# Optimization experiments

Measured on AMD Instinct MI355X. Metric: run time of the kernel, lower is better.

The kernel has to match this reference:

```python
import jax, jax.numpy as jnp
import numpy as np

BLOCK_SIZE = 4
CHANNEL_USE = 7
SAMPS = 20  # samps_per_symb in the original forward
LEAK = 0.01  # nn.LeakyReLU default slope


def _make_filters(K=101):
    # Deterministic stand-ins for h_lowpass.txt / h_pulseshape.txt
    n = np.arange(K) - (K - 1) / 2
    fc = 1.0 / SAMPS
    h_lp = (np.sinc(2 * fc * n) * np.hamming(K) * 2 * fc).astype(np.float32)
    h_ps = (np.sinc(n / SAMPS) * np.hamming(K)).astype(np.float32)
    return h_lp, h_ps


def _conv_same(sig, h):
    # Batched equivalent of np.convolve(row, h, 'same') for odd-length h.
    # sig: [N, L] float, h: [K] float. True convolution => flip kernel for lax correlation.
    K = h.shape[0]
    pad = (K - 1) // 2
    out = jax.lax.conv_general_dilated(
        sig[:, None, :], h[::-1][None, None, :],
        window_strides=(1,), padding=[(pad, pad)],
        dimension_numbers=('NCH', 'OIH', 'NCH'))
    return out[:, 0, :]


def setup_inputs() -> dict:
    key = jax.random.key(0)
    B, IN, CD = 131072, 16, 7
    ks = jax.random.split(key, 6)

    def lin(k, fi, fo):
        bound = 1.0 / np.sqrt(fi)
        kw, kb = jax.random.split(k)
        W = jax.random.uniform(kw, (fo, fi), jnp.float32, -bound, bound)
        b = jax.random.uniform(kb, (fo,), jnp.float32, -bound, bound)
        return W, b

    We1, be1 = lin(ks[0], IN, IN)
    We2, be2 = lin(ks[1], IN, CD)
    Wd1, bd1 = lin(ks[2], CD, IN)
    Wd2, bd2 = lin(ks[3], IN, IN)
    x = jax.random.normal(ks[4], (B, IN), jnp.float32)
    noise = jax.random.normal(ks[5], (B, CD), jnp.float32)
    h_lp, h_ps = _make_filters()
    return dict(x=x, We1=We1, be1=be1, We2=We2, be2=be2,
                Wd1=Wd1, bd1=bd1, Wd2=Wd2, bd2=bd2,
                h_lowpass=jnp.asarray(h_lp), h_pulseshape=jnp.asarray(h_ps),
                noise=noise, snr=4)


def reference(x, We1, be1, We2, be2, Wd1, bd1, Wd2, bd2,
              h_lowpass, h_pulseshape, noise, snr):
    B = x.shape[0]
    # ---- encoder MLP + global-norm scaling to power 70 ----
    h = jnp.dot(x, We1.T) + be1
    h = jnp.where(h >= 0, h, LEAK * h)
    enc = jnp.dot(h, We2.T) + be2
    enc = enc / jnp.linalg.norm(enc) * 70.0

    CD = enc.shape[1]          # bits_per_code
    M = 2 ** CD                # PSK order

    # ---- non-differentiable PSK channel (torch does .cpu().detach()) ----
    e = jax.lax.stop_gradient(enc)
    xi = jnp.round(e).astype(jnp.int32)           # int(np.round(.)) per element
    sign = jnp.where(xi < 0, -1.0, 1.0)           # sign_mask
    idx = jnp.mod(jnp.abs(xi), M)                  # bin() drops sign; values < M in practice
    phase = (2.0 * jnp.pi / M) * idx.astype(jnp.float32)
    sr, si = jnp.cos(phase), jnp.sin(phase)        # commpy PSK constellation exp(2*pi*i/M)

    def up(s):  # zero-stuff upsample by SAMPS: [B, CD] -> [B, CD*SAMPS]
        u = jnp.zeros((B, CD, SAMPS), s.dtype).at[:, :, 0].set(s)
        return u.reshape(B, CD * SAMPS)

    sig = jnp.concatenate([up(sr), up(si)], axis=0)  # real/imag stacked: [2B, L]
    sig = _conv_same(sig, h_pulseshape)
    sig = _conv_same(sig, h_lowpass)
    sig = _conv_same(sig, h_pulseshape)
    y = sig[:, ::SAMPS] * SAMPS                      # downsample, [2B, CD]
    yr, yi = y[:B], y[B:]
    # hard PSK demod = nearest unit-circle point = phase quantization
    ang = jnp.arctan2(yi, yr)
    idx_hat = jnp.mod(jnp.round(ang * (M / (2.0 * jnp.pi))), M)
    res = idx_hat.astype(jnp.float32) * sign

    # ---- AWGN ----
    rate = BLOCK_SIZE / CHANNEL_USE
    snr_lin = 10.0 ** (0.1 * snr)
    res = res + noise / jnp.sqrt(jnp.float32(2.0 * rate * snr_lin))

    # ---- decoder MLP ----
    d = jnp.dot(res, Wd1.T) + bd1
    d = jnp.where(d >= 0, d, LEAK * d)
    out = jnp.dot(d, Wd2.T) + bd2
    return out
```

## Files before the change

### kernel.cpp

```cpp
#include <hip/hip_runtime.h>
#include <math.h>

#define IN_DIM   16
#define CD       7
#define SAMPS    20
#define KFILT    101
#define SIGLEN   140
#define MCONST   128


__device__ __forceinline__ unsigned ld_u32(const void* p) {
    return __hip_atomic_load((const unsigned*)p, __ATOMIC_RELAXED,
                             __HIP_MEMORY_SCOPE_AGENT);
}
__device__ __forceinline__ void st_u32(void* p, unsigned v) {
    __hip_atomic_store((unsigned*)p, v, __ATOMIC_RELAXED,
                       __HIP_MEMORY_SCOPE_AGENT);
}
__device__ __forceinline__ unsigned add_u32(void* p) {
    return __hip_atomic_fetch_add((unsigned*)p, 1u, __ATOMIC_RELAXED,
                                  __HIP_MEMORY_SCOPE_AGENT);
}
__device__ __forceinline__ double ld_f64(const void* p) {
    return __hip_atomic_load((const double*)p, __ATOMIC_RELAXED,
                             __HIP_MEMORY_SCOPE_AGENT);
}
__device__ __forceinline__ void st_f64(void* p, double v) {
    __hip_atomic_store((double*)p, v, __ATOMIC_RELAXED,
                       __HIP_MEMORY_SCOPE_AGENT);
}
__device__ __forceinline__ float ld_f32(const void* p) {
    return __hip_atomic_load((const float*)p, __ATOMIC_RELAXED,
                             __HIP_MEMORY_SCOPE_AGENT);
}
__device__ __forceinline__ void st_f32(void* p, float v) {
    __hip_atomic_store((float*)p, v, __ATOMIC_RELAXED,
                       __HIP_MEMORY_SCOPE_AGENT);
}

__global__ __launch_bounds__(256, 2) void k_fused(
    const float* __restrict__ x,
    const float* __restrict__ We1, const float* __restrict__ be1,
    const float* __restrict__ We2, const float* __restrict__ be2,
    const float* __restrict__ Wd1, const float* __restrict__ bd1,
    const float* __restrict__ Wd2, const float* __restrict__ bd2,
    const float* __restrict__ h_lp, const float* __restrict__ h_ps,
    const float* __restrict__ noise, const int* __restrict__ snr_p,
    char* __restrict__ ws, float* __restrict__ out, int B, int NB)
{
    int t   = threadIdx.x;
    int bid = blockIdx.x;
    int row = bid * 256 + t;

    double* partials = (double*)(ws + 0);
    float*  GR       = (float*) (ws + 4096);
    char*   L0       = ws + 8192;
    char*   GS       = ws + 10240;
    char*   ROOT     = ws + 12288;
    char*   FLAG     = ws + 12544;

    __shared__ float    sW1[256], sW2[112], sb1[16], sb2[7];
    __shared__ float    sV1[112], sV2[256], sc1[16], sc2[16];
    __shared__ float    str[2 * MCONST];
    __shared__ float    snz[256 * CD];
    __shared__ double   wred[4];
    __shared__ float    sG[49];
    __shared__ float    curp[240], nxtp[240];
    __shared__ float    hA[KFILT], hB[KFILT];
    __shared__ unsigned sNormBits;
    __shared__ float    ninv;

    sW1[t] = We1[t];  sV2[t] = Wd2[t];
    if (t < 112) { sW2[t] = We2[t]; sV1[t] = Wd1[t]; }
    if (t < 16)  { sb1[t] = be1[t]; sc1[t] = bd1[t]; sc2[t] = bd2[t]; }
    if (t < 7)   sb2[t] = be2[t];
    if (bid < CD && t < KFILT) { hA[t] = h_ps[t]; hB[t] = h_lp[t]; }
    if (t < MCONST) {
        float ph = (float)(2.0 * 3.14159265358979323846 / (double)MCONST) * (float)t;
        str[t]          = cosf(ph);
        str[MCONST + t] = sinf(ph);
    }
    __syncthreads();

    float e[CD];
    double ss = 0.0;
    if (row < B) {
        const float4* xp = reinterpret_cast<const float4*>(x + (size_t)row * IN_DIM);
        float4 v0 = xp[0], v1 = xp[1], v2 = xp[2], v3 = xp[3];
        float xr[16] = {v0.x,v0.y,v0.z,v0.w, v1.x,v1.y,v1.z,v1.w,
                        v2.x,v2.y,v2.z,v2.w, v3.x,v3.y,v3.z,v3.w};
        float h[16];
        #pragma unroll
        for (int i = 0; i < 16; ++i) {
            float acc = sb1[i];
            #pragma unroll
            for (int j = 0; j < 16; ++j) acc = fmaf(sW1[i*16+j], xr[j], acc);
            h[i] = (acc >= 0.f) ? acc : 0.01f * acc;
        }
        #pragma unroll
        for (int o = 0; o < CD; ++o) {
            float acc = sb2[o];
            #pragma unroll
            for (int i = 0; i < 16; ++i) acc = fmaf(sW2[o*16+i], h[i], acc);
            e[o] = acc;
            ss += (double)acc * (double)acc;
        }
    }
    double v = ss;
    #pragma unroll
    for (int off = 32; off > 0; off >>= 1) v += __shfl_down(v, off);
    if ((t & 63) == 0) wred[t >> 6] = v;
    __syncthreads();
    if (t == 0) st_f64(&partials[bid], (wred[0] + wred[1]) + (wred[2] + wred[3]));

    if (bid < CD) {
        if (t < 240) { curp[t] = 0.0f; nxtp[t] = 0.0f; }
        __syncthreads();
        if (t < SIGLEN) {
            int m = t + 50 - SAMPS * bid;
            curp[t + 50] = (m >= 0 && m < KFILT) ? hA[m] : 0.0f;
        }
        __syncthreads();
        for (int f = 0; f < 2; ++f) {
            const float* h = (f == 0) ? hB : hA;
            if (t < SIGLEN) {
                float a0 = 0.f, a1 = 0.f;
                for (int m = 0; m <= 50; ++m)    a0 = fmaf(h[m], curp[t + 100 - m], a0);
                for (int m = 51; m < KFILT; ++m) a1 = fmaf(h[m], curp[t + 100 - m], a1);
                nxtp[t + 50] = a0 + a1;
            }
            __syncthreads();
            if (t < SIGLEN) curp[t + 50] = nxtp[t + 50];
            __syncthreads();
        }
        if (t < CD) {
            float gv = (float)SAMPS * curp[t * SAMPS + 50];
            #pragma unroll
            for (int r = 0; r < 8; ++r)
                st_f32(&GR[r * 64 + t * CD + bid], gv);
        }
    }

    {
        size_t nb  = (size_t)bid * (256 * CD);
        size_t lim = (size_t)B * CD;
        for (int i = t; i < 256 * CD; i += 256)
            if (nb + i < lim) snz[i] = noise[nb + i];
    }
    if (t == 1) {
        int iv = *snr_p;
        float sv = (iv >= -1000 && iv <= 1000) ? (float)iv
                                               : *reinterpret_cast<const float*>(snr_p);
        float snr_lin = powf(10.0f, 0.1f * sv);
        ninv = 1.0f / sqrtf((float)(8.0 / 7.0) * snr_lin);
    }

    __syncthreads();
    if (t < 64) {
        asm volatile("s_waitcnt vmcnt(0)" ::: "memory");
        int g       = bid >> 6;
        int gbase   = g << 6;
        int gsize   = (NB - gbase < 64) ? (NB - gbase) : 64;
        int ngroups = (NB + 63) >> 6;

        unsigned aret = 0;
        if (t == 0) aret = add_u32(L0 + (size_t)g * 256);
        aret = __shfl(aret, 0);
        if ((int)aret == gsize - 1) {
            double p = (t < gsize) ? ld_f64(&partials[gbase + t]) : 0.0;
            #pragma unroll
            for (int off = 32; off > 0; off >>= 1) p += __shfl_down(p, off);
            unsigned rret = 0;
            if (t == 0) {
                st_f64(GS + (size_t)g * 256, p);
                asm volatile("s_waitcnt vmcnt(0)" ::: "memory");
                rret = add_u32(ROOT);
            }
            rret = __shfl(rret, 0);
            if ((int)rret == ngroups - 1) {
                double gsv = (t < ngroups) ? ld_f64(GS + (size_t)t * 256) : 0.0;
                #pragma unroll
                for (int off = 32; off > 0; off >>= 1) gsv += __shfl_down(gsv, off);
                unsigned bits = 0;
                if (t == 0) bits = __float_as_uint((float)sqrt(gsv));
                bits = __shfl(bits, 0);
                if (t < 8) st_u32(FLAG + (size_t)t * 256, bits);
            }
        }
        if (t == 0) {
            unsigned b2;
            while ((b2 = ld_u32(FLAG + (size_t)(bid & 7) * 256)) == 0u)
                __builtin_amdgcn_s_sleep(4);
            sNormBits = b2;
        }
        if (t < 49) sG[t] = ld_f32(&GR[(size_t)(bid & 7) * 64 + t]);
    }
    __syncthreads();
    float sinv = 70.0f / __uint_as_float(sNormBits);

    if (row >= B) return;

    float sr[CD], si[CD], sgn[CD];
    #pragma unroll
    for (int o = 0; o < CD; ++o) {
        float es = e[o] * sinv;
        float rv = rintf(es);
        int xi = (int)rv;
        sgn[o] = (xi < 0) ? -1.0f : 1.0f;
        int idx = (xi < 0 ? -xi : xi) & (MCONST - 1);
        sr[o] = str[idx];
        si[o] = str[MCONST + idx];
    }

    float res[CD];
    #pragma unroll
    for (int k = 0; k < CD; ++k) {
        float yr = 0.f, yi = 0.f;
        #pragma unroll
        for (int cc = 0; cc < CD; ++cc) {
            float g = sG[k * CD + cc];
            yr = fmaf(g, sr[cc], yr);
            yi = fmaf(g, si[cc], yi);
        }
        float ang = atan2f(yi, yr);
        float q = ang * (float)(128.0 / (2.0 * 3.14159265358979323846));
        float r = rintf(q);
        float m = (r < 0.0f) ? r + 128.0f : r;
        res[k] = fmaf(snz[t * CD + k], ninv, m * sgn[k]);
    }

    float dd[16];
    #pragma unroll
    for (int i = 0; i < 16; ++i) {
        float acc = sc1[i];
        #pragma unroll
        for (int cc = 0; cc < CD; ++cc) acc = fmaf(sV1[i*CD+cc], res[cc], acc);
        dd[i] = (acc >= 0.f) ? acc : 0.01f * acc;
    }
    float4* op = reinterpret_cast<float4*>(out + (size_t)row * IN_DIM);
    #pragma unroll
    for (int q4 = 0; q4 < 4; ++q4) {
        float o0[4];
        #pragma unroll
        for (int u = 0; u < 4; ++u) {
            int i = q4 * 4 + u;
            float acc = sc2[i];
            #pragma unroll
            for (int j = 0; j < 16; ++j) acc = fmaf(sV2[i*16+j], dd[j], acc);
            o0[u] = acc;
        }
        op[q4] = make_float4(o0[0], o0[1], o0[2], o0[3]);
    }
}

__global__ __launch_bounds__(256) void k1_enc(
    const float* __restrict__ x,
    const float* __restrict__ We1, const float* __restrict__ be1,
    const float* __restrict__ We2, const float* __restrict__ be2,
    const float* __restrict__ h_lp, const float* __restrict__ h_ps,
    float* __restrict__ enc, double* __restrict__ partials,
    float* __restrict__ Gd, int B)
{
    int t = threadIdx.x, bid = blockIdx.x, row = bid * 256 + t;
    __shared__ float  sW1[256], sW2[112], sb1[16], sb2[7];
    __shared__ double wred[4];
    __shared__ float  curp[240], nxtp[240];
    __shared__ float  hA[KFILT], hB[KFILT];
    sW1[t] = We1[t];
    if (t < 112) sW2[t] = We2[t];
    if (t < 16)  sb1[t] = be1[t];
    if (t < 7)   sb2[t] = be2[t];
    if (bid < CD && t < KFILT) { hA[t] = h_ps[t]; hB[t] = h_lp[t]; }
    __syncthreads();
    double ss = 0.0;
    if (row < B) {
        const float4* xp = reinterpret_cast<const float4*>(x + (size_t)row * IN_DIM);
        float4 v0 = xp[0], v1 = xp[1], v2 = xp[2], v3 = xp[3];
        float xr[16] = {v0.x,v0.y,v0.z,v0.w, v1.x,v1.y,v1.z,v1.w,
                        v2.x,v2.y,v2.z,v2.w, v3.x,v3.y,v3.z,v3.w};
        float h[16];
        #pragma unroll
        for (int i = 0; i < 16; ++i) {
            float acc = sb1[i];
            #pragma unroll
            for (int j = 0; j < 16; ++j) acc = fmaf(sW1[i*16+j], xr[j], acc);
            h[i] = (acc >= 0.f) ? acc : 0.01f * acc;
        }
        float e[8];
        #pragma unroll
        for (int o = 0; o < CD; ++o) {
            float acc = sb2[o];
            #pragma unroll
            for (int i = 0; i < 16; ++i) acc = fmaf(sW2[o*16+i], h[i], acc);
            e[o] = acc; ss += (double)acc * (double)acc;
        }
        e[7] = 0.f;
        float4* ep = reinterpret_cast<float4*>(enc + (size_t)row * 8);
        ep[0] = make_float4(e[0], e[1], e[2], e[3]);
        ep[1] = make_float4(e[4], e[5], e[6], e[7]);
    }
    double v = ss;
    #pragma unroll
    for (int off = 32; off > 0; off >>= 1) v += __shfl_down(v, off);
    if ((t & 63) == 0) wred[t >> 6] = v;
    __syncthreads();
    if (t == 0) partials[bid] = (wred[0] + wred[1]) + (wred[2] + wred[3]);
    if (bid < CD) {
        if (t < 240) { curp[t] = 0.0f; nxtp[t] = 0.0f; }
        __syncthreads();
        if (t < SIGLEN) {
            int m = t + 50 - SAMPS * bid;
            curp[t + 50] = (m >= 0 && m < KFILT) ? hA[m] : 0.0f;
        }
        __syncthreads();
        for (int f = 0; f < 2; ++f) {
            const float* h = (f == 0) ? hB : hA;
            if (t < SIGLEN) {
                float a0 = 0.f, a1 = 0.f;
                for (int m = 0; m <= 50; ++m)    a0 = fmaf(h[m], curp[t + 100 - m], a0);
                for (int m = 51; m < KFILT; ++m) a1 = fmaf(h[m], curp[t + 100 - m], a1);
                nxtp[t + 50] = a0 + a1;
            }
            __syncthreads();
            if (t < SIGLEN) curp[t + 50] = nxtp[t + 50];
            __syncthreads();
        }
        if (t < CD) Gd[t * CD + bid] = (float)SAMPS * curp[t * SAMPS + 50];
    }
}

__global__ __launch_bounds__(256) void k2_main(
    const float* __restrict__ enc,
    const float* __restrict__ Wd1, const float* __restrict__ bd1,
    const float* __restrict__ Wd2, const float* __restrict__ bd2,
    const float* __restrict__ noise, const int* __restrict__ snr_p,
    const double* __restrict__ partials, const float* __restrict__ Gd,
    float* __restrict__ out, int B, int NBP)
{
    int t = threadIdx.x, bid = blockIdx.x, base_row = bid * 512;
    __shared__ float  sV1[112], sc1[16], sV2[256], sc2[16];
    __shared__ float  str[2 * MCONST];
    __shared__ float  sG[49];
    __shared__ double wred[4];
    __shared__ float  snz[512 * CD];
    __shared__ float  sinv, ninv;
    sV2[t] = Wd2[t];
    if (t < 112) sV1[t] = Wd1[t];
    if (t < 16)  { sc1[t] = bd1[t]; sc2[t] = bd2[t]; }
    if (t < 49)  sG[t] = Gd[t];
    if (t < MCONST) {
        float ph = (float)(2.0 * 3.14159265358979323846 / (double)MCONST) * (float)t;
        str[t] = cosf(ph); str[MCONST + t] = sinf(ph);
    }
    {
        size_t nb = (size_t)base_row * CD, lim = (size_t)B * CD;
        for (int i = t; i < 512 * CD; i += 256)
            if (nb + i < lim) snz[i] = noise[nb + i];
    }
    {
        double s = 0.0;
        for (int i = t; i < NBP; i += 256) s += partials[i];
        #pragma unroll
        for (int off = 32; off > 0; off >>= 1) s += __shfl_down(s, off);
        if ((t & 63) == 0) wred[t >> 6] = s;
    }
    __syncthreads();
    if (t == 0) sinv = 70.0f / (float)sqrt((wred[0] + wred[1]) + (wred[2] + wred[3]));
    if (t == 1) {
        int iv = *snr_p;
        float sv = (iv >= -1000 && iv <= 1000) ? (float)iv
                                               : *reinterpret_cast<const float*>(snr_p);
        float snr_lin = powf(10.0f, 0.1f * sv);
        ninv = 1.0f / sqrtf((float)(8.0 / 7.0) * snr_lin);
    }
    __syncthreads();
    #pragma unroll
    for (int c = 0; c < 2; ++c) {
        int lrow = c * 256 + t, row = base_row + lrow;
        if (row >= B) continue;
        const float4* ep = reinterpret_cast<const float4*>(enc + (size_t)row * 8);
        float4 e0 = ep[0], e1 = ep[1];
        float ev[7] = {e0.x, e0.y, e0.z, e0.w, e1.x, e1.y, e1.z};
        float sr[CD], si[CD], sgn[CD];
        #pragma unroll
        for (int o = 0; o < CD; ++o) {
            float es = ev[o] * sinv;
            float rv = rintf(es);
            int xi = (int)rv;
            sgn[o] = (xi < 0) ? -1.0f : 1.0f;
            int idx = (xi < 0 ? -xi : xi) & (MCONST - 1);
            sr[o] = str[idx]; si[o] = str[MCONST + idx];
        }
        float res[CD];
        #pragma unroll
        for (int k = 0; k < CD; ++k) {
            float yr = 0.f, yi = 0.f;
            #pragma unroll
            for (int cc = 0; cc < CD; ++cc) {
                float g = sG[k * CD + cc];
                yr = fmaf(g, sr[cc], yr); yi = fmaf(g, si[cc], yi);
            }
            float ang = atan2f(yi, yr);
            float q = ang * (float)(128.0 / (2.0 * 3.14159265358979323846));
            float r = rintf(q);
            float m = (r < 0.0f) ? r + 128.0f : r;
            res[k] = fmaf(snz[lrow * CD + k], ninv, m * sgn[k]);
        }
        float dd[16];
        #pragma unroll
        for (int i = 0; i < 16; ++i) {
            float acc = sc1[i];
            #pragma unroll
            for (int cc = 0; cc < CD; ++cc) acc = fmaf(sV1[i*CD+cc], res[cc], acc);
            dd[i] = (acc >= 0.f) ? acc : 0.01f * acc;
        }
        float4* op = reinterpret_cast<float4*>(out + (size_t)row * IN_DIM);
        #pragma unroll
        for (int q4 = 0; q4 < 4; ++q4) {
            float o0[4];
            #pragma unroll
            for (int u = 0; u < 4; ++u) {
                int i = q4 * 4 + u;
                float acc = sc2[i];
                #pragma unroll
                for (int j = 0; j < 16; ++j) acc = fmaf(sV2[i*16+j], dd[j], acc);
                o0[u] = acc;
            }
            op[q4] = make_float4(o0[0], o0[1], o0[2], o0[3]);
        }
    }
}

extern "C" void kernel_launch(void* const* d_in, const int* in_sizes, int n_in,
                              void* d_out, int out_size, void* d_ws, size_t ws_size,
                              hipStream_t stream)
{
    const float* x    = (const float*)d_in[0];
    const float* We1  = (const float*)d_in[1];
    const float* be1  = (const float*)d_in[2];
    const float* We2  = (const float*)d_in[3];
    const float* be2  = (const float*)d_in[4];
    const float* Wd1  = (const float*)d_in[5];
    const float* bd1  = (const float*)d_in[6];
    const float* Wd2  = (const float*)d_in[7];
    const float* bd2  = (const float*)d_in[8];
    const float* h_lp = (const float*)d_in[9];
    const float* h_ps = (const float*)d_in[10];
    const float* noise= (const float*)d_in[11];
    const int*   snr  = (const int*)d_in[12];
    float* out = (float*)d_out;

    int B  = in_sizes[0] / IN_DIM;
    int NB = (B + 255) / 256;

    char* ws = (char*)d_ws;

    if (NB <= 512) {
        hipMemsetAsync(ws + 8192, 0, 6400, stream);
        k_fused<<<NB, 256, 0, stream>>>(x, We1, be1, We2, be2, Wd1, bd1,
                                        Wd2, bd2, h_lp, h_ps, noise, snr,
                                        ws, out, B, NB);
    } else {
        double* partials = (double*)(ws + 0);
        float*  Gd       = (float*) (ws + 4096);
        float*  enc      = (float*) (ws + 16384);
        int NB2 = (B + 511) / 512;
        k1_enc<<<NB, 256, 0, stream>>>(x, We1, be1, We2, be2, h_lp, h_ps,
                                       enc, partials, Gd, B);
        k2_main<<<NB2, 256, 0, stream>>>(enc, Wd1, bd1, Wd2, bd2, noise, snr,
                                         partials, Gd, out, B, NB);
    }
}
```

Before: 28.95 us.

## Rotate received symbol by sent phase and use polynomial atan fast path

Noise is now loaded straight into registers per thread instead of being staged through a shared-memory buffer, which drops that LDS allocation and its store/load traffic. The demodulation rotates the received sample by the transmitted constellation point and, when the residual angle is small, computes it with a short odd polynomial instead of a full atan2f, falling back to atan2f otherwise. The spin-wait sleep interval is also halved. The polynomial path could round differently near quantization boundaries, and the per-thread strided 7-float noise loads may coalesce less well than the old block-wide copy.

```diff
diff --git a/kernel.cpp b/kernel.cpp
--- a/kernel.cpp
+++ b/kernel.cpp
@@ -62,7 +62,6 @@
     __shared__ float    sW1[256], sW2[112], sb1[16], sb2[7];
     __shared__ float    sV1[112], sV2[256], sc1[16], sc2[16];
     __shared__ float    str[2 * MCONST];
-    __shared__ float    snz[256 * CD];
     __shared__ double   wred[4];
     __shared__ float    sG[49];
     __shared__ float    curp[240], nxtp[240];
@@ -141,11 +140,14 @@
         }
     }
 
-    {
-        size_t nb  = (size_t)bid * (256 * CD);
-        size_t lim = (size_t)B * CD;
-        for (int i = t; i < 256 * CD; i += 256)
-            if (nb + i < lim) snz[i] = noise[nb + i];
+    float nz[CD];
+    if (row < B) {
+        const float* np0 = noise + (size_t)row * CD;
+        #pragma unroll
+        for (int k = 0; k < CD; ++k) nz[k] = np0[k];
+    } else {
+        #pragma unroll
+        for (int k = 0; k < CD; ++k) nz[k] = 0.f;
     }
     if (t == 1) {
         int iv = *snr_p;
@@ -190,7 +192,7 @@
         if (t == 0) {
             unsigned b2;
             while ((b2 = ld_u32(FLAG + (size_t)(bid & 7) * 256)) == 0u)
-                __builtin_amdgcn_s_sleep(4);
+                __builtin_amdgcn_s_sleep(2);
             sNormBits = b2;
         }
         if (t < 49) sG[t] = ld_f32(&GR[(size_t)(bid & 7) * 64 + t]);
@@ -200,7 +202,7 @@
 
     if (row >= B) return;
 
-    float sr[CD], si[CD], sgn[CD];
+    float sr[CD], si[CD], sgn[CD], fidx[CD];
     #pragma unroll
     for (int o = 0; o < CD; ++o) {
         float es = e[o] * sinv;
@@ -208,10 +210,12 @@
         int xi = (int)rv;
         sgn[o] = (xi < 0) ? -1.0f : 1.0f;
         int idx = (xi < 0 ? -xi : xi) & (MCONST - 1);
+        fidx[o] = (float)idx;
         sr[o] = str[idx];
         si[o] = str[MCONST + idx];
     }
 
+    const float QSC = 20.37183271576260f;
     float res[CD];
     #pragma unroll
     for (int k = 0; k < CD; ++k) {
@@ -222,11 +226,24 @@
             yr = fmaf(g, sr[cc], yr);
             yi = fmaf(g, si[cc], yi);
         }
-        float ang = atan2f(yi, yr);
-        float q = ang * (float)(128.0 / (2.0 * 3.14159265358979323846));
+        float c = sr[k], s = si[k];
+        float a = fmaf(yr, c, yi * s);
+        float b = fmaf(yi, c, -(yr * s));
+        float q;
+        if (fabsf(b) < 0.25f * a) {
+            float u  = b / a;
+            float u2 = u * u;
+            float w  = fmaf(u2, -0.142857143f, 0.2f);
+            w        = fmaf(u2, w, -0.333333333f);
+            w        = fmaf(u2, w, 1.0f);
+            q = fmaf(u * w, QSC, fidx[k]);
+        } else {
+            q = fmaf(atan2f(b, a), QSC, fidx[k]);
+        }
         float r = rintf(q);
-        float m = (r < 0.0f) ? r + 128.0f : r;
-        res[k] = fmaf(snz[t * CD + k], ninv, m * sgn[k]);
+        if (r < 0.0f) r += 128.0f;
+        else if (r >= 128.0f) r -= 128.0f;
+        res[k] = fmaf(nz[k], ninv, r * sgn[k]);
     }
 
     float dd[16];
```

Result: faster. 27.40 us, median of 2 (-5.4%).
